# Kernel optimization log

Measured on AMD Instinct MI355X. Metric: run time of the kernel, lower is better.

Reference implementation:

```python
import jax, jax.numpy as jnp
import numpy as np

N_NODES = 20000
N_EDGES = 100000
N_SNAP = 2
N_DIM, E_DIM, OUT_DIM, HEADS = 64, 32, 64, 2


def edge_gat(x, ef, src, dst, Wn, We, al, ar, ae, b):
    # DGL EdgeGATConv: fc (no bias), edge-aware attention, edge softmax over
    # incoming edges, message = (ft_src + ft_edge) * alpha, final additive bias.
    H, D = al.shape
    ft = (x @ Wn).reshape(-1, H, D)                # [N,H,D]
    fe = (ef @ We).reshape(-1, H, D)               # [E,H,D]
    el = jnp.einsum('nhd,hd->nh', ft, al)          # [N,H]
    er = jnp.einsum('nhd,hd->nh', ft, ar)          # [N,H]
    ee = jnp.einsum('ehd,hd->eh', fe, ae)          # [E,H]
    logits = jax.nn.leaky_relu(el[src] + er[dst] + ee, 0.2)  # [E,H]
    m = jax.ops.segment_max(logits, dst, num_segments=N_NODES)
    p = jnp.exp(logits - m[dst])
    s = jax.ops.segment_sum(p, dst, num_segments=N_NODES)
    a = p / s[dst]                                 # edge softmax per dst node
    msg = (ft[src] + fe) * a[..., None]            # [E,H,D]
    return jax.ops.segment_sum(msg, dst, num_segments=N_NODES) + b  # [N,H,D]


def gnn_rnn(x, ef, src, dst, params):
    # GNN_RNN.forward per snapshot: stacked EdgeGAT layers, head-mean each.
    for (Wn, We, al, ar, ae, b) in params:
        x = edge_gat(x, ef, src, dst, Wn, We, al, ar, ae, b).mean(axis=1)
    return x


def _mk_layer(key, in_d, e_d, out_d, heads, scale=0.1):
    ks = jax.random.split(key, 6)
    return dict(
        Wn=jax.random.normal(ks[0], (in_d, heads * out_d), jnp.float32) * scale,
        We=jax.random.normal(ks[1], (e_d, heads * out_d), jnp.float32) * scale,
        al=jax.random.normal(ks[2], (heads, out_d), jnp.float32) * scale,
        ar=jax.random.normal(ks[3], (heads, out_d), jnp.float32) * scale,
        ae=jax.random.normal(ks[4], (heads, out_d), jnp.float32) * scale,
        b=jax.random.normal(ks[5], (heads, out_d), jnp.float32) * scale,
    )


def setup_inputs() -> dict:
    key = jax.random.key(0)
    ks = jax.random.split(key, 10)
    inp = {
        'x': jax.random.normal(ks[0], (N_SNAP, N_NODES, N_DIM), jnp.float32),
        'e': jax.random.normal(ks[1], (N_SNAP, N_EDGES, E_DIM), jnp.float32),
        'src': jax.random.randint(ks[2], (N_SNAP, N_EDGES), 0, N_NODES),
        'dst': jax.random.randint(ks[3], (N_SNAP, N_EDGES), 0, N_NODES),
    }
    enc0 = _mk_layer(ks[4], N_DIM, E_DIM, OUT_DIM, HEADS)
    enc1 = _mk_layer(ks[5], OUT_DIM, E_DIM, OUT_DIM, HEADS)
    dec0 = _mk_layer(ks[6], OUT_DIM, E_DIM, N_DIM, HEADS)
    dec1 = _mk_layer(ks[7], N_DIM, E_DIM, N_DIM, HEADS)
    for pref, lp in [('enc0', enc0), ('enc1', enc1), ('dec0', dec0), ('dec1', dec1)]:
        for k, v in lp.items():
            inp[f'{pref}_{k}'] = v
    inp['W_e2d'] = jax.random.normal(ks[8], (OUT_DIM, OUT_DIM), jnp.float32) * 0.1
    return inp


def reference(x, e, src, dst,
              enc0_Wn, enc0_We, enc0_al, enc0_ar, enc0_ae, enc0_b,
              enc1_Wn, enc1_We, enc1_al, enc1_ar, enc1_ae, enc1_b,
              W_e2d,
              dec0_Wn, dec0_We, dec0_al, dec0_ar, dec0_ae, dec0_b,
              dec1_Wn, dec1_We, dec1_al, dec1_ar, dec1_ae, dec1_b):
    enc_params = [(enc0_Wn, enc0_We, enc0_al, enc0_ar, enc0_ae, enc0_b),
                  (enc1_Wn, enc1_We, enc1_al, enc1_ar, enc1_ae, enc1_b)]
    dec_params = [(dec0_Wn, dec0_We, dec0_al, dec0_ar, dec0_ae, dec0_b),
                  (dec1_Wn, dec1_We, dec1_al, dec1_ar, dec1_ae, dec1_b)]

    def per_snapshot(xs, es, ss, ds):
        h = gnn_rnn(xs, es, ss, ds, enc_params)   # encoder, [N,out_dim]
        h = h @ W_e2d.T                           # encoder_to_decoder (no bias)
        return gnn_rnn(h, es, ss, ds, dec_params) # decoder, [N,n_dim]

    decoded = jax.vmap(per_snapshot)(x, e, src, dst)  # [S,N,n_dim]
    return decoded[-1]
```

## Files before the change

kernel.cpp:

```cpp
#include <hip/hip_runtime.h>
#include <math.h>

#define N_NODES 20000
#define N_EDGES 100000

__device__ __forceinline__ float rl_f(float v, int l) {
    return __uint_as_float(__builtin_amdgcn_readlane(__float_as_uint(v), l));
}
__device__ __forceinline__ int rl_i(int v, int l) {
    return __builtin_amdgcn_readlane(v, l);
}
__device__ __forceinline__ float lrelu(float x) { return x > 0.f ? x : 0.2f * x; }

__global__ __launch_bounds__(256) void scan_kernel(const int* __restrict__ cnt,
                                                   int* __restrict__ row_ptr) {
    __shared__ int sdata[256];
    __shared__ int swsum[4];
    const int tid = threadIdx.x;
    const int b = blockIdx.x;
    int idx = b * 256 + tid;
    int v = (idx < N_NODES) ? cnt[idx] : 0;
    sdata[tid] = v;
    int partial = 0;
    for (int i = tid; i < b * 256; i += 256) partial += cnt[i];
#pragma unroll
    for (int off = 32; off; off >>= 1) partial += __shfl_xor(partial, off);
    if ((tid & 63) == 0) swsum[tid >> 6] = partial;
    __syncthreads();
    const int boff = swsum[0] + swsum[1] + swsum[2] + swsum[3];
    for (int off = 1; off < 256; off <<= 1) {
        int t_ = (tid >= off) ? sdata[tid - off] : 0;
        __syncthreads();
        sdata[tid] += t_;
        __syncthreads();
    }
    if (idx < N_NODES) row_ptr[idx] = boff + sdata[tid] - v;
    if (b == 0 && tid == 0) row_ptr[N_NODES] = N_EDGES;
}

__global__ __launch_bounds__(256) void setup_kernel(
    const int* __restrict__ dst, int* __restrict__ cnt, int* __restrict__ pos,
    const float* __restrict__ Wn0, const float* __restrict__ al0, const float* __restrict__ ar0,
    const float* __restrict__ Wn1, const float* __restrict__ al1, const float* __restrict__ ar1,
    const float* __restrict__ dWn, const float* __restrict__ al2, const float* __restrict__ ar2,
    const float* __restrict__ Wn3, const float* __restrict__ al3, const float* __restrict__ ar3,
    const float* __restrict__ W_e2d,
    const float* __restrict__ We0, const float* __restrict__ ae0,
    const float* __restrict__ We1, const float* __restrict__ ae1,
    const float* __restrict__ We2, const float* __restrict__ ae2,
    const float* __restrict__ We3, const float* __restrict__ ae3,
    const float* __restrict__ X0,
    float* __restrict__ P4, float* __restrict__ Q, float4* __restrict__ Wpack,
    float2* __restrict__ EL2, float2* __restrict__ ER2) {
    __shared__ float praw[256];
    const int t = threadIdx.x;
    const int bb = blockIdx.x;

    if (bb < 391) {
        int e = bb * 256 + t;
        if (e < N_EDGES) pos[e] = atomicAdd(&cnt[dst[e]], 1);
        return;
    }
    const int b = bb - 391;

    if (b < 4) {
        const int L = b;
        if (L != 2) {
            const float* Wn = (L == 0) ? Wn0 : (L == 1) ? Wn1 : Wn3;
            const float* al = (L == 0) ? al0 : (L == 1) ? al1 : al3;
            const float* ar = (L == 0) ? ar0 : (L == 1) ? ar1 : ar3;
            const int k = t >> 2, o = t & 3;
            const float* a = (o & 2) ? ar : al;
            const int h = o & 1;
            float acc = 0.f;
#pragma unroll 8
            for (int d = 0; d < 64; d++) acc = fmaf(Wn[k * 128 + h * 64 + d], a[h * 64 + d], acc);
            P4[L * 256 + t] = acc;
        } else {
            {
                const int i = t >> 2, o = t & 3;
                const float* a = (o & 2) ? ar2 : al2;
                const int h = o & 1;
                float acc = 0.f;
#pragma unroll 8
                for (int d = 0; d < 64; d++) acc = fmaf(dWn[i * 128 + h * 64 + d], a[h * 64 + d], acc);
                praw[t] = acc;
            }
            __syncthreads();
            const int j = t >> 2, o = t & 3;
            float acc = 0.f;
#pragma unroll 8
            for (int i = 0; i < 64; i++) acc = fmaf(W_e2d[i * 64 + j], praw[i * 4 + o], acc);
            P4[2 * 256 + t] = acc;
        }
    } else if (b == 4) {
        const int k = t >> 3, o = t & 7, L = o >> 1, h = o & 1;
        const float* We = (L == 0) ? We0 : (L == 1) ? We1 : (L == 2) ? We2 : We3;
        const float* ae = (L == 0) ? ae0 : (L == 1) ? ae1 : (L == 2) ? ae2 : ae3;
        float acc = 0.f;
#pragma unroll 8
        for (int d = 0; d < 64; d++) acc = fmaf(We[k * 128 + h * 64 + d], ae[h * 64 + d], acc);
        Q[t] = acc;
    } else if (b < 53) {
        const int idx = (b - 5) * 256 + t;
        const int L = idx / 3072;
        const int sub = idx - L * 3072;
        if (sub < 2048) {
            const int k2 = sub >> 6, l = sub & 63;
            if (L != 2) {
                const float* Wn = (L == 0) ? Wn0 : (L == 1) ? Wn1 : Wn3;
                Wpack[idx] = make_float4(Wn[(2 * k2) * 128 + l], Wn[(2 * k2) * 128 + 64 + l],
                                         Wn[(2 * k2 + 1) * 128 + l], Wn[(2 * k2 + 1) * 128 + 64 + l]);
            } else {
                float a0 = 0.f, a1 = 0.f, a2 = 0.f, a3 = 0.f;
#pragma unroll 4
                for (int i = 0; i < 64; i++) {
                    float wa = W_e2d[i * 64 + 2 * k2], wb = W_e2d[i * 64 + 2 * k2 + 1];
                    float da = dWn[i * 128 + l], db = dWn[i * 128 + 64 + l];
                    a0 = fmaf(wa, da, a0);
                    a1 = fmaf(wa, db, a1);
                    a2 = fmaf(wb, da, a2);
                    a3 = fmaf(wb, db, a3);
                }
                Wpack[idx] = make_float4(a0, a1, a2, a3);
            }
        } else {
            const int s2 = sub - 2048;
            const int k2 = s2 >> 6, l = s2 & 63;
            const float* We = (L == 0) ? We0 : (L == 1) ? We1 : (L == 2) ? We2 : We3;
            Wpack[idx] = make_float4(We[(2 * k2) * 128 + l], We[(2 * k2) * 128 + 64 + l],
                                     We[(2 * k2 + 1) * 128 + l], We[(2 * k2 + 1) * 128 + 64 + l]);
        }
    } else {
        {
            const int k = t >> 2, o = t & 3;
            const float* a = (o & 2) ? ar0 : al0;
            const int h = o & 1;
            float acc = 0.f;
#pragma unroll 8
            for (int d = 0; d < 64; d++) acc = fmaf(Wn0[k * 128 + h * 64 + d], a[h * 64 + d], acc);
            praw[t] = acc;
        }
        __syncthreads();
        const int lane = t & 63;
        const int wave = t >> 6;
        const float px = praw[lane * 4 + 0], py = praw[lane * 4 + 1];
        const float pz = praw[lane * 4 + 2], pw = praw[lane * 4 + 3];
        const int nb = (int)gridDim.x - 444;
        for (int node = (b - 53) * 4 + wave; node < N_NODES; node += nb * 4) {
            float xv = X0[node * 64 + lane];
            float e0 = xv * px, e1 = xv * py, f0 = xv * pz, f1 = xv * pw;
#pragma unroll
            for (int off = 32; off; off >>= 1) {
                e0 += __shfl_xor(e0, off);
                e1 += __shfl_xor(e1, off);
                f0 += __shfl_xor(f0, off);
                f1 += __shfl_xor(f1, off);
            }
            if (lane == 0) {
                EL2[node] = make_float2(e0, e1);
                ER2[node] = make_float2(f0, f1);
            }
        }
    }
}

__global__ __launch_bounds__(256) void prep_kernel(const float* __restrict__ Efeat,
                                                   const int* __restrict__ src,
                                                   const int* __restrict__ dst,
                                                   const int* __restrict__ pos,
                                                   const int* __restrict__ row_ptr,
                                                   const float* __restrict__ Q,
                                                   float* __restrict__ E_csr,
                                                   int* __restrict__ src_csr,
                                                   float* __restrict__ EE_csr) {
    __shared__ float QS[256];
    __shared__ float ES[32][33];
    __shared__ int JS[32];
    const int tid = threadIdx.x;
    QS[tid] = Q[tid];
    const int e0 = blockIdx.x * 32;
    const int el_ = tid >> 3, quad = tid & 7;
    float4 v = ((const float4*)Efeat)[(size_t)(e0 + el_) * 8 + quad];
    ES[el_][quad * 4 + 0] = v.x;
    ES[el_][quad * 4 + 1] = v.y;
    ES[el_][quad * 4 + 2] = v.z;
    ES[el_][quad * 4 + 3] = v.w;
    if (tid < 32) {
        int e = e0 + tid;
        int j = row_ptr[dst[e]] + pos[e];
        JS[tid] = j;
        src_csr[j] = src[e];
    }
    __syncthreads();
    const int j = JS[el_];
    ((float4*)E_csr)[(size_t)j * 8 + quad] = v;
    const int o = quad;
    float acc = 0.f;
#pragma unroll
    for (int k = 0; k < 32; k++) acc = fmaf(ES[el_][k], QS[k * 8 + o], acc);
    EE_csr[(size_t)(o >> 1) * 2 * N_EDGES + (size_t)j * 2 + (o & 1)] = acc;
}

__device__ __forceinline__ void gather_one(
    int beg, int end, float2 er,
    const float* __restrict__ X, const float* __restrict__ E_csr,
    const int* __restrict__ src_csr, const float2* __restrict__ ELi,
    const float2* __restrict__ EE_L,
    int lane, int half, int hl,
    float& ax0, float& ax1, float& aeh) {
    ax0 = 0.f; ax1 = 0.f; aeh = 0.f;
    const int deg = end - beg;
    if (deg == 0) return;
    float l0 = 0.f, l1 = 0.f, aX0 = 0.f, aX1 = 0.f, aE = 0.f;
    if (deg <= 64) {
        int sn = 0;
        float w0 = 0.f, w1 = 0.f;
        if (lane < deg) {
            sn = src_csr[beg + lane];
            float2 ee = EE_L[beg + lane];
            float2 el = ELi[sn];
            w0 = __expf(lrelu(el.x + er.x + ee.x));
            w1 = __expf(lrelu(el.y + er.y + ee.y));
        }
        l0 = w0; l1 = w1;
#pragma unroll
        for (int off = 32; off; off >>= 1) {
            l0 += __shfl_xor(l0, off);
            l1 += __shfl_xor(l1, off);
        }
        const int dm1 = deg - 1;
        {
            float xs[8], es[8];
#pragma unroll
            for (int t = 0; t < 8; t++) {
                int ct = t < dm1 ? t : dm1;
                int st = rl_i(sn, ct);
                xs[t] = X[st * 64 + lane];
                es[t] = E_csr[(size_t)(beg + ct) * 32 + hl];
            }
#pragma unroll
            for (int t = 0; t < 8; t++) {
                float w0t = rl_f(w0, t);
                float w1t = rl_f(w1, t);
                aX0 = fmaf(w0t, xs[t], aX0);
                aX1 = fmaf(w1t, xs[t], aX1);
                aE = fmaf(half ? w1t : w0t, es[t], aE);
            }
        }
        int t = 8;
        for (; t + 4 <= deg; t += 4) {
            int s0 = rl_i(sn, t), s1 = rl_i(sn, t + 1);
            int s2 = rl_i(sn, t + 2), s3 = rl_i(sn, t + 3);
            float x0 = X[s0 * 64 + lane];
            float x1 = X[s1 * 64 + lane];
            float x2 = X[s2 * 64 + lane];
            float x3 = X[s3 * 64 + lane];
            const float* Eb = E_csr + (size_t)(beg + t) * 32 + hl;
            float e0 = Eb[0], e1 = Eb[32], e2 = Eb[64], e3 = Eb[96];
            float w00 = rl_f(w0, t), w01 = rl_f(w0, t + 1);
            float w02 = rl_f(w0, t + 2), w03 = rl_f(w0, t + 3);
            float w10 = rl_f(w1, t), w11 = rl_f(w1, t + 1);
            float w12 = rl_f(w1, t + 2), w13 = rl_f(w1, t + 3);
            aX0 = fmaf(w00, x0, aX0); aX1 = fmaf(w10, x0, aX1);
            aX0 = fmaf(w01, x1, aX0); aX1 = fmaf(w11, x1, aX1);
            aX0 = fmaf(w02, x2, aX0); aX1 = fmaf(w12, x2, aX1);
            aX0 = fmaf(w03, x3, aX0); aX1 = fmaf(w13, x3, aX1);
            aE = fmaf(half ? w10 : w00, e0, aE);
            aE = fmaf(half ? w11 : w01, e1, aE);
            aE = fmaf(half ? w12 : w02, e2, aE);
            aE = fmaf(half ? w13 : w03, e3, aE);
        }
        for (; t < deg; t++) {
            int st = rl_i(sn, t);
            float w0t = rl_f(w0, t), w1t = rl_f(w1, t);
            float xv = X[st * 64 + lane];
            float ev = E_csr[(size_t)(beg + t) * 32 + hl];
            aX0 = fmaf(w0t, xv, aX0);
            aX1 = fmaf(w1t, xv, aX1);
            aE = fmaf(half ? w1t : w0t, ev, aE);
        }
    } else {
        for (int c = beg; c < end; c += 64) {
            int jj = c + lane;
            int sn_ = 0;
            float w0c = 0.f, w1c = 0.f;
            if (jj < end) {
                sn_ = src_csr[jj];
                float2 ee = EE_L[jj];
                float2 el = ELi[sn_];
                w0c = __expf(lrelu(el.x + er.x + ee.x));
                w1c = __expf(lrelu(el.y + er.y + ee.y));
            }
            float s0_ = w0c, s1_ = w1c;
#pragma unroll
            for (int off = 32; off; off >>= 1) {
                s0_ += __shfl_xor(s0_, off);
                s1_ += __shfl_xor(s1_, off);
            }
            l0 += s0_;
            l1 += s1_;
            int nch = (end - c) < 64 ? (end - c) : 64;
            for (int t = 0; t < nch; t++) {
                int st = rl_i(sn_, t);
                float w0t = rl_f(w0c, t), w1t = rl_f(w1c, t);
                float xv = X[st * 64 + lane];
                float ev = E_csr[(size_t)(c + t) * 32 + hl];
                aX0 = fmaf(w0t, xv, aX0);
                aX1 = fmaf(w1t, xv, aX1);
                aE = fmaf(half ? w1t : w0t, ev, aE);
            }
        }
    }
    const float inv0 = l0 > 0.f ? 1.f / l0 : 0.f;
    const float inv1 = l1 > 0.f ? 1.f / l1 : 0.f;
    ax0 = aX0 * inv0;
    ax1 = aX1 * inv1;
    aeh = aE * (half ? inv1 : inv0);
}

__global__ __launch_bounds__(256) void layer_kernel(
    const float* __restrict__ X,
    const float2* __restrict__ ELi, const float2* __restrict__ ERi,
    const float* __restrict__ E_csr, const int* __restrict__ src_csr,
    const int* __restrict__ row_ptr, const float2* __restrict__ EE_L,
    const float4* __restrict__ Wp, const float* __restrict__ bias,
    const float* __restrict__ P4next, const int has_next,
    float* __restrict__ OUT,
    float2* __restrict__ ELo, float2* __restrict__ ERo) {
    __shared__ float4 WS[2048];
    __shared__ float4 BC4[256];
    __shared__ float2 AE2[256];
    const int tid = threadIdx.x;
    const int lane = tid & 63;
    const int wave = tid >> 6;
    const int half = lane >> 5, hl = lane & 31;
    const int wb = wave * 64;

    const int n0 = blockIdx.x * 8 + wave * 2;
    const int n1 = n0 + 1;
    const int beg0 = row_ptr[n0];
    const int beg1 = row_ptr[n1];
    const int end1 = row_ptr[n1 + 1];
    const float2 er0 = ERi[n0];
    const float2 er1 = ERi[n1];
    const float bb0 = bias[lane], bb1 = bias[64 + lane];
    const float4 p = has_next ? ((const float4*)P4next)[lane] : make_float4(0.f, 0.f, 0.f, 0.f);

#pragma unroll
    for (int i = 0; i < 8; i++) WS[i * 256 + tid] = Wp[i * 256 + tid];
    const float4* __restrict__ WeG = Wp + 2048;
    __syncthreads();

    const int end0 = beg1;
    const int deg0 = end0 - beg0;
    const int deg1 = end1 - beg1;

    float ax0a = 0.f, ax1a = 0.f, aeha = 0.f;
    float ax0b = 0.f, ax1b = 0.f, aehb = 0.f;

    if (deg0 > 0 && deg0 <= 64 && deg1 > 0 && deg1 <= 64) {
        int sn0 = 0, sn1 = 0;
        float w0a = 0.f, w1a = 0.f, w0b = 0.f, w1b = 0.f;
        if (lane < deg0) {
            sn0 = src_csr[beg0 + lane];
            float2 ee = EE_L[beg0 + lane];
            float2 el = ELi[sn0];
            w0a = __expf(lrelu(el.x + er0.x + ee.x));
            w1a = __expf(lrelu(el.y + er0.y + ee.y));
        }
        if (lane < deg1) {
            sn1 = src_csr[beg1 + lane];
            float2 ee = EE_L[beg1 + lane];
            float2 el = ELi[sn1];
            w0b = __expf(lrelu(el.x + er1.x + ee.x));
            w1b = __expf(lrelu(el.y + er1.y + ee.y));
        }
        BC4[wb + lane] = make_float4(w0a, w1a, w0b, w1b);
        float l0a = w0a, l1a = w1a, l0b = w0b, l1b = w1b;
#pragma unroll
        for (int off = 32; off; off >>= 1) {
            l0a += __shfl_xor(l0a, off);
            l1a += __shfl_xor(l1a, off);
            l0b += __shfl_xor(l0b, off);
            l1b += __shfl_xor(l1b, off);
        }
        float aX0a = 0.f, aX1a = 0.f, aEa = 0.f;
        float aX0b = 0.f, aX1b = 0.f, aEb = 0.f;
        const int dma = deg0 - 1, dmb = deg1 - 1;
        {
            float xs0[8], es0[8], xs1[8], es1[8];
#pragma unroll
            for (int t = 0; t < 8; t++) {
                int c0 = t < dma ? t : dma;
                int c1 = t < dmb ? t : dmb;
                int s0 = rl_i(sn0, c0);
                int s1 = rl_i(sn1, c1);
                xs0[t] = X[s0 * 64 + lane];
                es0[t] = E_csr[(size_t)(beg0 + c0) * 32 + hl];
                xs1[t] = X[s1 * 64 + lane];
                es1[t] = E_csr[(size_t)(beg1 + c1) * 32 + hl];
            }
#pragma unroll
            for (int t = 0; t < 8; t++) {
                float4 wt = BC4[wb + t];
                aX0a = fmaf(wt.x, xs0[t], aX0a);
                aX1a = fmaf(wt.y, xs0[t], aX1a);
                aEa = fmaf(half ? wt.y : wt.x, es0[t], aEa);
                aX0b = fmaf(wt.z, xs1[t], aX0b);
                aX1b = fmaf(wt.w, xs1[t], aX1b);
                aEb = fmaf(half ? wt.w : wt.z, es1[t], aEb);
            }
        }
        int t = 8;
        for (; t + 4 <= deg0; t += 4) {
            int s0 = rl_i(sn0, t), s1 = rl_i(sn0, t + 1);
            int s2 = rl_i(sn0, t + 2), s3 = rl_i(sn0, t + 3);
            float x0 = X[s0 * 64 + lane];
            float x1 = X[s1 * 64 + lane];
            float x2 = X[s2 * 64 + lane];
            float x3 = X[s3 * 64 + lane];
            const float* Eb = E_csr + (size_t)(beg0 + t) * 32 + hl;
            float e0 = Eb[0], e1 = Eb[32], e2 = Eb[64], e3 = Eb[96];
            float4 wt0 = BC4[wb + t], wt1 = BC4[wb + t + 1];
            float4 wt2 = BC4[wb + t + 2], wt3 = BC4[wb + t + 3];
            aX0a = fmaf(wt0.x, x0, aX0a); aX1a = fmaf(wt0.y, x0, aX1a);
            aX0a = fmaf(wt1.x, x1, aX0a); aX1a = fmaf(wt1.y, x1, aX1a);
            aX0a = fmaf(wt2.x, x2, aX0a); aX1a = fmaf(wt2.y, x2, aX1a);
            aX0a = fmaf(wt3.x, x3, aX0a); aX1a = fmaf(wt3.y, x3, aX1a);
            aEa = fmaf(half ? wt0.y : wt0.x, e0, aEa);
            aEa = fmaf(half ? wt1.y : wt1.x, e1, aEa);
            aEa = fmaf(half ? wt2.y : wt2.x, e2, aEa);
            aEa = fmaf(half ? wt3.y : wt3.x, e3, aEa);
        }
        for (; t < deg0; t++) {
            int st = rl_i(sn0, t);
            float4 wt = BC4[wb + t];
            float xv = X[st * 64 + lane];
            float ev = E_csr[(size_t)(beg0 + t) * 32 + hl];
            aX0a = fmaf(wt.x, xv, aX0a);
            aX1a = fmaf(wt.y, xv, aX1a);
            aEa = fmaf(half ? wt.y : wt.x, ev, aEa);
        }
        t = 8;
        for (; t + 4 <= deg1; t += 4) {
            int s0 = rl_i(sn1, t), s1 = rl_i(sn1, t + 1);
            int s2 = rl_i(sn1, t + 2), s3 = rl_i(sn1, t + 3);
            float x0 = X[s0 * 64 + lane];
            float x1 = X[s1 * 64 + lane];
            float x2 = X[s2 * 64 + lane];
            float x3 = X[s3 * 64 + lane];
            const float* Eb = E_csr + (size_t)(beg1 + t) * 32 + hl;
            float e0 = Eb[0], e1 = Eb[32], e2 = Eb[64], e3 = Eb[96];
            float4 wt0 = BC4[wb + t], wt1 = BC4[wb + t + 1];
            float4 wt2 = BC4[wb + t + 2], wt3 = BC4[wb + t + 3];
            aX0b = fmaf(wt0.z, x0, aX0b); aX1b = fmaf(wt0.w, x0, aX1b);
            aX0b = fmaf(wt1.z, x1, aX0b); aX1b = fmaf(wt1.w, x1, aX1b);
            aX0b = fmaf(wt2.z, x2, aX0b); aX1b = fmaf(wt2.w, x2, aX1b);
            aX0b = fmaf(wt3.z, x3, aX0b); aX1b = fmaf(wt3.w, x3, aX1b);
            aEb = fmaf(half ? wt0.w : wt0.z, e0, aEb);
            aEb = fmaf(half ? wt1.w : wt1.z, e1, aEb);
            aEb = fmaf(half ? wt2.w : wt2.z, e2, aEb);
            aEb = fmaf(half ? wt3.w : wt3.z, e3, aEb);
        }
        for (; t < deg1; t++) {
            int st = rl_i(sn1, t);
            float4 wt = BC4[wb + t];
            float xv = X[st * 64 + lane];
            float ev = E_csr[(size_t)(beg1 + t) * 32 + hl];
            aX0b = fmaf(wt.z, xv, aX0b);
            aX1b = fmaf(wt.w, xv, aX1b);
            aEb = fmaf(half ? wt.w : wt.z, ev, aEb);
        }
        const float i0a = l0a > 0.f ? 1.f / l0a : 0.f;
        const float i1a = l1a > 0.f ? 1.f / l1a : 0.f;
        const float i0b = l0b > 0.f ? 1.f / l0b : 0.f;
        const float i1b = l1b > 0.f ? 1.f / l1b : 0.f;
        ax0a = aX0a * i0a; ax1a = aX1a * i1a; aeha = aEa * (half ? i1a : i0a);
        ax0b = aX0b * i0b; ax1b = aX1b * i1b; aehb = aEb * (half ? i1b : i0b);
    } else {
        gather_one(beg0, end0, er0, X, E_csr, src_csr, ELi, EE_L, lane, half, hl,
                   ax0a, ax1a, aeha);
        gather_one(beg1, end1, er1, X, E_csr, src_csr, ELi, EE_L, lane, half, hl,
                   ax0b, ax1b, aehb);
    }

    BC4[wb + lane] = make_float4(ax0a, ax1a, ax0b, ax1b);
    AE2[wb + lane] = make_float2(aeha, aehb);

    float r0a = 0.f, r1a = 0.f, r0b = 0.f, r1b = 0.f;
#pragma unroll
    for (int k2 = 0; k2 < 32; k2++) {
        float4 w4 = WS[k2 * 64 + lane];
        float4 a0 = BC4[wb + 2 * k2];
        float4 a1 = BC4[wb + 2 * k2 + 1];
        r0a = fmaf(a0.x, w4.x, r0a); r1a = fmaf(a0.y, w4.y, r1a);
        r0a = fmaf(a1.x, w4.z, r0a); r1a = fmaf(a1.y, w4.w, r1a);
        r0b = fmaf(a0.z, w4.x, r0b); r1b = fmaf(a0.w, w4.y, r1b);
        r0b = fmaf(a1.z, w4.z, r0b); r1b = fmaf(a1.w, w4.w, r1b);
    }
#pragma unroll
    for (int k2 = 0; k2 < 16; k2++) {
        float4 w4 = WeG[k2 * 64 + lane];
        float2 e0 = AE2[wb + 2 * k2];
        float2 e1 = AE2[wb + 2 * k2 + 1];
        float2 e2 = AE2[wb + 32 + 2 * k2];
        float2 e3 = AE2[wb + 32 + 2 * k2 + 1];
        r0a = fmaf(e0.x, w4.x, r0a); r1a = fmaf(e2.x, w4.y, r1a);
        r0a = fmaf(e1.x, w4.z, r0a); r1a = fmaf(e3.x, w4.w, r1a);
        r0b = fmaf(e0.y, w4.x, r0b); r1b = fmaf(e2.y, w4.y, r1b);
        r0b = fmaf(e1.y, w4.z, r0b); r1b = fmaf(e3.y, w4.w, r1b);
    }
    const float outa = 0.5f * (r0a + bb0 + r1a + bb1);
    const float outb = 0.5f * (r0b + bb0 + r1b + bb1);
    OUT[n0 * 64 + lane] = outa;
    OUT[n1 * 64 + lane] = outb;
    if (has_next) {
        float e0a = outa * p.x, e1a = outa * p.y, f0a = outa * p.z, f1a = outa * p.w;
        float e0b = outb * p.x, e1b = outb * p.y, f0b = outb * p.z, f1b = outb * p.w;
#pragma unroll
        for (int off = 32; off; off >>= 1) {
            e0a += __shfl_xor(e0a, off); e1a += __shfl_xor(e1a, off);
            f0a += __shfl_xor(f0a, off); f1a += __shfl_xor(f1a, off);
            e0b += __shfl_xor(e0b, off); e1b += __shfl_xor(e1b, off);
            f0b += __shfl_xor(f0b, off); f1b += __shfl_xor(f1b, off);
        }
        if (lane == 0) {
            ELo[n0] = make_float2(e0a, e1a);
            ERo[n0] = make_float2(f0a, f1a);
            ELo[n1] = make_float2(e0b, e1b);
            ERo[n1] = make_float2(f0b, f1b);
        }
    }
}

extern "C" void kernel_launch(void* const* d_in, const int* in_sizes, int n_in,
                              void* d_out, int out_size, void* d_ws, size_t ws_size,
                              hipStream_t stream) {
    const float* x = (const float*)d_in[0];
    const float* e = (const float*)d_in[1];
    const int* src = (const int*)d_in[2];
    const int* dst = (const int*)d_in[3];

    const float* x1 = x + (size_t)1 * N_NODES * 64;
    const float* e1 = e + (size_t)1 * N_EDGES * 32;
    const int* src1 = src + N_EDGES;
    const int* dst1 = dst + N_EDGES;

    int we2d_idx, dec0_b, dec1_b;
    if (in_sizes[16] == 64 * 64 && in_sizes[17] == 64 * 128) {
        we2d_idx = 16; dec0_b = 17; dec1_b = 23;
    } else {
        dec0_b = 16; dec1_b = 22; we2d_idx = 28;
    }
    auto P = [&](int i) { return (const float*)d_in[i]; };

    char* ws = (char*)d_ws;
    int* cnt      = (int*)(ws + 0);
    int* row_ptr  = (int*)(ws + 80000);
    int* pos      = (int*)(ws + 160064);
    float* q      = (float*)(ws + 560576);
    int* src_csr  = (int*)(ws + 561600);
    float* e_csr  = (float*)(ws + 961600);
    float* ee_csr = (float*)(ws + 13761600);
    float* p4_all = (float*)(ws + 16961600);
    float* elA    = (float*)(ws + 16965696);
    float* erA    = (float*)(ws + 17125696);
    float* elB    = (float*)(ws + 17285696);
    float* erB    = (float*)(ws + 17445696);
    float* h0     = (float*)(ws + 17605696);
    float* h1     = (float*)(ws + 22725696);
    float4* wpack = (float4*)(ws + 27845696);

    hipMemsetAsync(cnt, 0, N_NODES * sizeof(int), stream);

    setup_kernel<<<903, 256, 0, stream>>>(
        dst1, cnt, pos,
        P(4), P(6), P(7),
        P(10), P(12), P(13),
        P(dec0_b + 0), P(dec0_b + 2), P(dec0_b + 3),
        P(dec1_b + 0), P(dec1_b + 2), P(dec1_b + 3),
        P(we2d_idx),
        P(5), P(8), P(11), P(14),
        P(dec0_b + 1), P(dec0_b + 4), P(dec1_b + 1), P(dec1_b + 4),
        x1,
        p4_all, q, wpack, (float2*)elA, (float2*)erA);

    const int SB = (N_NODES + 255) / 256;
    scan_kernel<<<SB, 256, 0, stream>>>(cnt, row_ptr);

    prep_kernel<<<N_EDGES / 32, 256, 0, stream>>>(e1, src1, dst1, pos, row_ptr, q,
                                                  e_csr, src_csr, ee_csr);

    const int NB_L = N_NODES / 8;
    auto run = [&](const float* Xin, int L, const float* bias_,
                   const float* elI, const float* erI,
                   float* Out, float* elO, float* erO, int hn) {
        layer_kernel<<<NB_L, 256, 0, stream>>>(
            Xin, (const float2*)elI, (const float2*)erI,
            e_csr, src_csr, row_ptr,
            (const float2*)ee_csr + (size_t)L * N_EDGES,
            wpack + (size_t)L * 3072, bias_,
            p4_all + (L + 1) * 256, hn,
            Out, (float2*)elO, (float2*)erO);
    };

    run(x1, 0, P(9),           elA, erA, h0, elB, erB, 1);
    run(h0, 1, P(15),          elB, erB, h1, elA, erA, 1);
    run(h1, 2, P(dec0_b + 5),  elA, erA, h0, elB, erB, 1);
    run(h0, 3, P(dec1_b + 5),  elB, erB, (float*)d_out, elA, erA, 0);
}
```

Baseline: 267.8 us.

## Process four destination nodes per wave in layer kernel

Each wave now handles four destination nodes instead of two, halving the block count and amortizing the per-block shared-memory load of the packed weight matrix over twice as many nodes. The weight reads from shared memory in the projection loop are reused across four node accumulators. The 4-wide unrolled remainder loops were replaced by simple scalar loops. Register pressure rises and per-wave latency grows, and the fast path now requires all four nodes to have degree 1..64.

```diff
diff --git a/kernel.cpp b/kernel.cpp
--- a/kernel.cpp
+++ b/kernel.cpp
@@ -329,21 +329,22 @@
     float* __restrict__ OUT,
     float2* __restrict__ ELo, float2* __restrict__ ERo) {
     __shared__ float4 WS[2048];
-    __shared__ float4 BC4[256];
-    __shared__ float2 AE2[256];
+    __shared__ float4 BC4[512];
+    __shared__ float4 AE4[256];
     const int tid = threadIdx.x;
     const int lane = tid & 63;
     const int wave = tid >> 6;
     const int half = lane >> 5, hl = lane & 31;
-    const int wb = wave * 64;
-
-    const int n0 = blockIdx.x * 8 + wave * 2;
-    const int n1 = n0 + 1;
-    const int beg0 = row_ptr[n0];
-    const int beg1 = row_ptr[n1];
-    const int end1 = row_ptr[n1 + 1];
+    const int wbA = wave * 64;
+    const int wbB = 256 + wave * 64;
+
+    const int n0 = blockIdx.x * 16 + wave * 4;
+    const int4 rp = *(const int4*)(row_ptr + n0);
+    const int end3 = row_ptr[n0 + 4];
     const float2 er0 = ERi[n0];
-    const float2 er1 = ERi[n1];
+    const float2 er1 = ERi[n0 + 1];
+    const float2 er2 = ERi[n0 + 2];
+    const float2 er3 = ERi[n0 + 3];
     const float bb0 = bias[lane], bb1 = bias[64 + lane];
     const float4 p = has_next ? ((const float4*)P4next)[lane] : make_float4(0.f, 0.f, 0.f, 0.f);
 
@@ -352,43 +353,65 @@
     const float4* __restrict__ WeG = Wp + 2048;
     __syncthreads();
 
-    const int end0 = beg1;
-    const int deg0 = end0 - beg0;
-    const int deg1 = end1 - beg1;
+    const int beg0 = rp.x, beg1 = rp.y, beg2 = rp.z, beg3 = rp.w;
+    const int d0 = beg1 - beg0, d1 = beg2 - beg1, d2 = beg3 - beg2, d3 = end3 - beg3;
 
     float ax0a = 0.f, ax1a = 0.f, aeha = 0.f;
     float ax0b = 0.f, ax1b = 0.f, aehb = 0.f;
-
-    if (deg0 > 0 && deg0 <= 64 && deg1 > 0 && deg1 <= 64) {
-        int sn0 = 0, sn1 = 0;
+    float ax0c = 0.f, ax1c = 0.f, aehc = 0.f;
+    float ax0d = 0.f, ax1d = 0.f, aehd = 0.f;
+
+    const bool fast = (d0 > 0) & (d0 <= 64) & (d1 > 0) & (d1 <= 64) &
+                      (d2 > 0) & (d2 <= 64) & (d3 > 0) & (d3 <= 64);
+    if (fast) {
+        int sn0 = 0, sn1 = 0, sn2 = 0, sn3 = 0;
         float w0a = 0.f, w1a = 0.f, w0b = 0.f, w1b = 0.f;
-        if (lane < deg0) {
+        float w0c = 0.f, w1c = 0.f, w0d = 0.f, w1d = 0.f;
+        if (lane < d0) {
             sn0 = src_csr[beg0 + lane];
             float2 ee = EE_L[beg0 + lane];
             float2 el = ELi[sn0];
             w0a = __expf(lrelu(el.x + er0.x + ee.x));
             w1a = __expf(lrelu(el.y + er0.y + ee.y));
         }
-        if (lane < deg1) {
+        if (lane < d1) {
             sn1 = src_csr[beg1 + lane];
             float2 ee = EE_L[beg1 + lane];
             float2 el = ELi[sn1];
             w0b = __expf(lrelu(el.x + er1.x + ee.x));
             w1b = __expf(lrelu(el.y + er1.y + ee.y));
         }
-        BC4[wb + lane] = make_float4(w0a, w1a, w0b, w1b);
+        if (lane < d2) {
+            sn2 = src_csr[beg2 + lane];
+            float2 ee = EE_L[beg2 + lane];
+            float2 el = ELi[sn2];
+            w0c = __expf(lrelu(el.x + er2.x + ee.x));
+            w1c = __expf(lrelu(el.y + er2.y + ee.y));
+        }
+        if (lane < d3) {
+            sn3 = src_csr[beg3 + lane];
+            float2 ee = EE_L[beg3 + lane];
+            float2 el = ELi[sn3];
+            w0d = __expf(lrelu(el.x + er3.x + ee.x));
+            w1d = __expf(lrelu(el.y + er3.y + ee.y));
+        }
+        BC4[wbA + lane] = make_float4(w0a, w1a, w0b, w1b);
+        BC4[wbB + lane] = make_float4(w0c, w1c, w0d, w1d);
         float l0a = w0a, l1a = w1a, l0b = w0b, l1b = w1b;
+        float l0c = w0c, l1c = w1c, l0d = w0d, l1d = w1d;
 #pragma unroll
         for (int off = 32; off; off >>= 1) {
-            l0a += __shfl_xor(l0a, off);
-            l1a += __shfl_xor(l1a, off);
-            l0b += __shfl_xor(l0b, off);
-            l1b += __shfl_xor(l1b, off);
+            l0a += __shfl_xor(l0a, off); l1a += __shfl_xor(l1a, off);
+            l0b += __shfl_xor(l0b, off); l1b += __shfl_xor(l1b, off);
+            l0c += __shfl_xor(l0c, off); l1c += __shfl_xor(l1c, off);
+            l0d += __shfl_xor(l0d, off); l1d += __shfl_xor(l1d, off);
         }
         float aX0a = 0.f, aX1a = 0.f, aEa = 0.f;
         float aX0b = 0.f, aX1b = 0.f, aEb = 0.f;
-        const int dma = deg0 - 1, dmb = deg1 - 1;
+        float aX0c = 0.f, aX1c = 0.f, aEc = 0.f;
+        float aX0d = 0.f, aX1d = 0.f, aEd = 0.f;
         {
+            const int dma = d0 - 1, dmb = d1 - 1;
             float xs0[8], es0[8], xs1[8], es1[8];
 #pragma unroll
             for (int t = 0; t < 8; t++) {
@@ -403,7 +426,7 @@
             }
 #pragma unroll
             for (int t = 0; t < 8; t++) {
-                float4 wt = BC4[wb + t];
+                float4 wt = BC4[wbA + t];
                 aX0a = fmaf(wt.x, xs0[t], aX0a);
                 aX1a = fmaf(wt.y, xs0[t], aX1a);
                 aEa = fmaf(half ? wt.y : wt.x, es0[t], aEa);
@@ -412,124 +435,161 @@
                 aEb = fmaf(half ? wt.w : wt.z, es1[t], aEb);
             }
         }
-        int t = 8;
-        for (; t + 4 <= deg0; t += 4) {
-            int s0 = rl_i(sn0, t), s1 = rl_i(sn0, t + 1);
-            int s2 = rl_i(sn0, t + 2), s3 = rl_i(sn0, t + 3);
-            float x0 = X[s0 * 64 + lane];
-            float x1 = X[s1 * 64 + lane];
-            float x2 = X[s2 * 64 + lane];
-            float x3 = X[s3 * 64 + lane];
-            const float* Eb = E_csr + (size_t)(beg0 + t) * 32 + hl;
-            float e0 = Eb[0], e1 = Eb[32], e2 = Eb[64], e3 = Eb[96];
-            float4 wt0 = BC4[wb + t], wt1 = BC4[wb + t + 1];
-            float4 wt2 = BC4[wb + t + 2], wt3 = BC4[wb + t + 3];
-            aX0a = fmaf(wt0.x, x0, aX0a); aX1a = fmaf(wt0.y, x0, aX1a);
-            aX0a = fmaf(wt1.x, x1, aX0a); aX1a = fmaf(wt1.y, x1, aX1a);
-            aX0a = fmaf(wt2.x, x2, aX0a); aX1a = fmaf(wt2.y, x2, aX1a);
-            aX0a = fmaf(wt3.x, x3, aX0a); aX1a = fmaf(wt3.y, x3, aX1a);
-            aEa = fmaf(half ? wt0.y : wt0.x, e0, aEa);
-            aEa = fmaf(half ? wt1.y : wt1.x, e1, aEa);
-            aEa = fmaf(half ? wt2.y : wt2.x, e2, aEa);
-            aEa = fmaf(half ? wt3.y : wt3.x, e3, aEa);
-        }
-        for (; t < deg0; t++) {
+        {
+            const int dmc = d2 - 1, dmd = d3 - 1;
+            float xs2[8], es2[8], xs3[8], es3[8];
+#pragma unroll
+            for (int t = 0; t < 8; t++) {
+                int c2 = t < dmc ? t : dmc;
+                int c3 = t < dmd ? t : dmd;
+                int s2 = rl_i(sn2, c2);
+                int s3 = rl_i(sn3, c3);
+                xs2[t] = X[s2 * 64 + lane];
+                es2[t] = E_csr[(size_t)(beg2 + c2) * 32 + hl];
+                xs3[t] = X[s3 * 64 + lane];
+                es3[t] = E_csr[(size_t)(beg3 + c3) * 32 + hl];
+            }
+#pragma unroll
+            for (int t = 0; t < 8; t++) {
+                float4 wt = BC4[wbB + t];
+                aX0c = fmaf(wt.x, xs2[t], aX0c);
+                aX1c = fmaf(wt.y, xs2[t], aX1c);
+                aEc = fmaf(half ? wt.y : wt.x, es2[t], aEc);
+                aX0d = fmaf(wt.z, xs3[t], aX0d);
+                aX1d = fmaf(wt.w, xs3[t], aX1d);
+                aEd = fmaf(half ? wt.w : wt.z, es3[t], aEd);
+            }
+        }
+        for (int t = 8; t < d0; t++) {
             int st = rl_i(sn0, t);
-            float4 wt = BC4[wb + t];
+            float4 wt = BC4[wbA + t];
             float xv = X[st * 64 + lane];
             float ev = E_csr[(size_t)(beg0 + t) * 32 + hl];
             aX0a = fmaf(wt.x, xv, aX0a);
             aX1a = fmaf(wt.y, xv, aX1a);
             aEa = fmaf(half ? wt.y : wt.x, ev, aEa);
         }
-        t = 8;
-        for (; t + 4 <= deg1; t += 4) {
-            int s0 = rl_i(sn1, t), s1 = rl_i(sn1, t + 1);
-            int s2 = rl_i(sn1, t + 2), s3 = rl_i(sn1, t + 3);
-            float x0 = X[s0 * 64 + lane];
-            float x1 = X[s1 * 64 + lane];
-            float x2 = X[s2 * 64 + lane];
-            float x3 = X[s3 * 64 + lane];
-            const float* Eb = E_csr + (size_t)(beg1 + t) * 32 + hl;
-            float e0 = Eb[0], e1 = Eb[32], e2 = Eb[64], e3 = Eb[96];
-            float4 wt0 = BC4[wb + t], wt1 = BC4[wb + t + 1];
-            float4 wt2 = BC4[wb + t + 2], wt3 = BC4[wb + t + 3];
-            aX0b = fmaf(wt0.z, x0, aX0b); aX1b = fmaf(wt0.w, x0, aX1b);
-            aX0b = fmaf(wt1.z, x1, aX0b); aX1b = fmaf(wt1.w, x1, aX1b);
-            aX0b = fmaf(wt2.z, x2, aX0b); aX1b = fmaf(wt2.w, x2, aX1b);
-            aX0b = fmaf(wt3.z, x3, aX0b); aX1b = fmaf(wt3.w, x3, aX1b);
-            aEb = fmaf(half ? wt0.w : wt0.z, e0, aEb);
-            aEb = fmaf(half ? wt1.w : wt1.z, e1, aEb);
-            aEb = fmaf(half ? wt2.w : wt2.z, e2, aEb);
-            aEb = fmaf(half ? wt3.w : wt3.z, e3, aEb);
-        }
-        for (; t < deg1; t++) {
+        for (int t = 8; t < d1; t++) {
             int st = rl_i(sn1, t);
-            float4 wt = BC4[wb + t];
+            float4 wt = BC4[wbA + t];
             float xv = X[st * 64 + lane];
             float ev = E_csr[(size_t)(beg1 + t) * 32 + hl];
             aX0b = fmaf(wt.z, xv, aX0b);
             aX1b = fmaf(wt.w, xv, aX1b);
             aEb = fmaf(half ? wt.w : wt.z, ev, aEb);
         }
+        for (int t = 8; t < d2; t++) {
+            int st = rl_i(sn2, t);
+            float4 wt = BC4[wbB + t];
+            float xv = X[st * 64 + lane];
+            float ev = E_csr[(size_t)(beg2 + t) * 32 + hl];
+            aX0c = fmaf(wt.x, xv, aX0c);
+            aX1c = fmaf(wt.y, xv, aX1c);
+            aEc = fmaf(half ? wt.y : wt.x, ev, aEc);
+        }
+        for (int t = 8; t < d3; t++) {
+            int st = rl_i(sn3, t);
+            float4 wt = BC4[wbB + t];
+            float xv = X[st * 64 + lane];
+            float ev = E_csr[(size_t)(beg3 + t) * 32 + hl];
+            aX0d = fmaf(wt.z, xv, aX0d);
+            aX1d = fmaf(wt.w, xv, aX1d);
+            aEd = fmaf(half ? wt.w : wt.z, ev, aEd);
+        }
         const float i0a = l0a > 0.f ? 1.f / l0a : 0.f;
         const float i1a = l1a > 0.f ? 1.f / l1a : 0.f;
         const float i0b = l0b > 0.f ? 1.f / l0b : 0.f;
         const float i1b = l1b > 0.f ? 1.f / l1b : 0.f;
+        const float i0c = l0c > 0.f ? 1.f / l0c : 0.f;
+        const float i1c = l1c > 0.f ? 1.f / l1c : 0.f;
+        const float i0d = l0d > 0.f ? 1.f / l0d : 0.f;
+        const float i1d = l1d > 0.f ? 1.f / l1d : 0.f;
         ax0a = aX0a * i0a; ax1a = aX1a * i1a; aeha = aEa * (half ? i1a : i0a);
         ax0b = aX0b * i0b; ax1b = aX1b * i1b; aehb = aEb * (half ? i1b : i0b);
+        ax0c = aX0c * i0c; ax1c = aX1c * i1c; aehc = aEc * (half ? i1c : i0c);
+        ax0d = aX0d * i0d; ax1d = aX1d * i1d; aehd = aEd * (half ? i1d : i0d);
     } else {
-        gather_one(beg0, end0, er0, X, E_csr, src_csr, ELi, EE_L, lane, half, hl,
+        gather_one(beg0, beg1, er0, X, E_csr, src_csr, ELi, EE_L, lane, half, hl,
                    ax0a, ax1a, aeha);
-        gather_one(beg1, end1, er1, X, E_csr, src_csr, ELi, EE_L, lane, half, hl,
+        gather_one(beg1, beg2, er1, X, E_csr, src_csr, ELi, EE_L, lane, half, hl,
                    ax0b, ax1b, aehb);
-    }
-
-    BC4[wb + lane] = make_float4(ax0a, ax1a, ax0b, ax1b);
-    AE2[wb + lane] = make_float2(aeha, aehb);
+        gather_one(beg2, beg3, er2, X, E_csr, src_csr, ELi, EE_L, lane, half, hl,
+                   ax0c, ax1c, aehc);
+        gather_one(beg3, end3, er3, X, E_csr, src_csr, ELi, EE_L, lane, half, hl,
+                   ax0d, ax1d, aehd);
+    }
+
+    BC4[wbA + lane] = make_float4(ax0a, ax1a, ax0b, ax1b);
+    BC4[wbB + lane] = make_float4(ax0c, ax1c, ax0d, ax1d);
+    AE4[wave * 64 + lane] = make_float4(aeha, aehb, aehc, aehd);
 
     float r0a = 0.f, r1a = 0.f, r0b = 0.f, r1b = 0.f;
+    float r0c = 0.f, r1c = 0.f, r0d = 0.f, r1d = 0.f;
 #pragma unroll
     for (int k2 = 0; k2 < 32; k2++) {
         float4 w4 = WS[k2 * 64 + lane];
-        float4 a0 = BC4[wb + 2 * k2];
-        float4 a1 = BC4[wb + 2 * k2 + 1];
+        float4 a0 = BC4[wbA + 2 * k2];
+        float4 a1 = BC4[wbA + 2 * k2 + 1];
+        float4 b0 = BC4[wbB + 2 * k2];
+        float4 b1 = BC4[wbB + 2 * k2 + 1];
         r0a = fmaf(a0.x, w4.x, r0a); r1a = fmaf(a0.y, w4.y, r1a);
         r0a = fmaf(a1.x, w4.z, r0a); r1a = fmaf(a1.y, w4.w, r1a);
         r0b = fmaf(a0.z, w4.x, r0b); r1b = fmaf(a0.w, w4.y, r1b);
         r0b = fmaf(a1.z, w4.z, r0b); r1b = fmaf(a1.w, w4.w, r1b);
+        r0c = fmaf(b0.x, w4.x, r0c); r1c = fmaf(b0.y, w4.y, r1c);
+        r0c = fmaf(b1.x, w4.z, r0c); r1c = fmaf(b1.y, w4.w, r1c);
+        r0d = fmaf(b0.z, w4.x, r0d); r1d = fmaf(b0.w, w4.y, r1d);
+        r0d = fmaf(b1.z, w4.z, r0d); r1d = fmaf(b1.w, w4.w, r1d);
     }
 #pragma unroll
     for (int k2 = 0; k2 < 16; k2++) {
         float4 w4 = WeG[k2 * 64 + lane];
-        float2 e0 = AE2[wb + 2 * k2];
-        float2 e1 = AE2[wb + 2 * k2 + 1];
-        float2 e2 = AE2[wb + 32 + 2 * k2];
-        float2 e3 = AE2[wb + 32 + 2 * k2 + 1];
+        float4 e0 = AE4[wave * 64 + 2 * k2];
+        float4 e1 = AE4[wave * 64 + 2 * k2 + 1];
+        float4 e2 = AE4[wave * 64 + 32 + 2 * k2];
+        float4 e3 = AE4[wave * 64 + 32 + 2 * k2 + 1];
         r0a = fmaf(e0.x, w4.x, r0a); r1a = fmaf(e2.x, w4.y, r1a);
         r0a = fmaf(e1.x, w4.z, r0a); r1a = fmaf(e3.x, w4.w, r1a);
         r0b = fmaf(e0.y, w4.x, r0b); r1b = fmaf(e2.y, w4.y, r1b);
         r0b = fmaf(e1.y, w4.z, r0b); r1b = fmaf(e3.y, w4.w, r1b);
+        r0c = fmaf(e0.z, w4.x, r0c); r1c = fmaf(e2.z, w4.y, r1c);
+        r0c = fmaf(e1.z, w4.z, r0c); r1c = fmaf(e3.z, w4.w, r1c);
+        r0d = fmaf(e0.w, w4.x, r0d); r1d = fmaf(e2.w, w4.y, r1d);
+        r0d = fmaf(e1.w, w4.z, r0d); r1d = fmaf(e3.w, w4.w, r1d);
     }
     const float outa = 0.5f * (r0a + bb0 + r1a + bb1);
     const float outb = 0.5f * (r0b + bb0 + r1b + bb1);
-    OUT[n0 * 64 + lane] = outa;
-    OUT[n1 * 64 + lane] = outb;
+    const float outc = 0.5f * (r0c + bb0 + r1c + bb1);
+    const float outd = 0.5f * (r0d + bb0 + r1d + bb1);
+    OUT[(n0 + 0) * 64 + lane] = outa;
+    OUT[(n0 + 1) * 64 + lane] = outb;
+    OUT[(n0 + 2) * 64 + lane] = outc;
+    OUT[(n0 + 3) * 64 + lane] = outd;
     if (has_next) {
         float e0a = outa * p.x, e1a = outa * p.y, f0a = outa * p.z, f1a = outa * p.w;
         float e0b = outb * p.x, e1b = outb * p.y, f0b = outb * p.z, f1b = outb * p.w;
+        float e0c = outc * p.x, e1c = outc * p.y, f0c = outc * p.z, f1c = outc * p.w;
+        float e0d = outd * p.x, e1d = outd * p.y, f0d = outd * p.z, f1d = outd * p.w;
 #pragma unroll
         for (int off = 32; off; off >>= 1) {
             e0a += __shfl_xor(e0a, off); e1a += __shfl_xor(e1a, off);
             f0a += __shfl_xor(f0a, off); f1a += __shfl_xor(f1a, off);
             e0b += __shfl_xor(e0b, off); e1b += __shfl_xor(e1b, off);
             f0b += __shfl_xor(f0b, off); f1b += __shfl_xor(f1b, off);
+            e0c += __shfl_xor(e0c, off); e1c += __shfl_xor(e1c, off);
+            f0c += __shfl_xor(f0c, off); f1c += __shfl_xor(f1c, off);
+            e0d += __shfl_xor(e0d, off); e1d += __shfl_xor(e1d, off);
+            f0d += __shfl_xor(f0d, off); f1d += __shfl_xor(f1d, off);
         }
         if (lane == 0) {
-            ELo[n0] = make_float2(e0a, e1a);
-            ERo[n0] = make_float2(f0a, f1a);
-            ELo[n1] = make_float2(e0b, e1b);
-            ERo[n1] = make_float2(f0b, f1b);
+            ELo[n0 + 0] = make_float2(e0a, e1a);
+            ERo[n0 + 0] = make_float2(f0a, f1a);
+            ELo[n0 + 1] = make_float2(e0b, e1b);
+            ERo[n0 + 1] = make_float2(f0b, f1b);
+            ELo[n0 + 2] = make_float2(e0c, e1c);
+            ERo[n0 + 2] = make_float2(f0c, f1c);
+            ELo[n0 + 3] = make_float2(e0d, e1d);
+            ERo[n0 + 3] = make_float2(f0d, f1d);
         }
     }
 }
@@ -592,7 +652,7 @@
     prep_kernel<<<N_EDGES / 32, 256, 0, stream>>>(e1, src1, dst1, pos, row_ptr, q,
                                                   e_csr, src_csr, ee_csr);
 
-    const int NB_L = N_NODES / 8;
+    const int NB_L = N_NODES / 16;
     auto run = [&](const float* Xin, int L, const float* bias_,
                    const float* elI, const float* erI,
                    float* Out, float* elO, float* erO, int hn) {
```

New measurement: 275.7 us. 1.03x slower.
